# Kernel tuning notes

Hardware: AMD Instinct MI355X
Metric: run time of the kernel (lower is better)

## Reference

```python
import jax, jax.numpy as jnp
import numpy as np

N = 30000        # entities
R_EFF = 9        # 2*r+1 after enrich() with r=4
F_IN = 256       # insize
HID = 256        # hidden
NCLS = 32        # numcls
BASES = 16
E = 500000       # number of (enriched) triples / nonzeros


def setup_inputs() -> dict:
    key = jax.random.key(0)
    ks = jax.random.split(key, 8)
    features = jax.random.normal(ks[0], (N, F_IN), dtype=jnp.float32)
    # sparse vertical adjacency: entry at (rel*N + dst, src)
    ver_rows = jax.random.randint(ks[1], (E,), 0, R_EFF * N, dtype=jnp.int32)
    ver_cols = jax.random.randint(ks[2], (E,), 0, N, dtype=jnp.int32)
    # row-sum normalization (sum_sparse in the original): vals = 1 / row_degree
    deg = jax.ops.segment_sum(jnp.ones((E,), jnp.float32), ver_rows,
                              num_segments=R_EFF * N)
    ver_vals = 1.0 / deg[ver_rows]
    # xavier-uniform-ish params
    def xavier(k, shape):
        fan_in, fan_out = shape[-2], shape[-1]
        lim = jnp.sqrt(6.0 / (fan_in + fan_out)) * jnp.sqrt(2.0)  # relu gain
        return jax.random.uniform(k, shape, jnp.float32, -lim, lim)
    comps1 = xavier(ks[3], (R_EFF, BASES))
    bases1 = xavier(ks[4], (BASES, F_IN, HID))
    comps2 = xavier(ks[5], (R_EFF, BASES))
    bases2 = xavier(ks[6], (BASES, HID, NCLS))
    bias1 = jnp.zeros((HID,), jnp.float32)
    bias2 = jnp.zeros((NCLS,), jnp.float32)
    return {"features": features, "ver_vals": ver_vals,
            "comps1": comps1, "bases1": bases1,
            "comps2": comps2, "bases2": bases2,
            "bias1": bias1, "bias2": bias2,
            "ver_rows": ver_rows, "ver_cols": ver_cols}


def _spmm(vals, rows, cols, x, num_rows):
    # sparse [num_rows, n] @ x [n, d] -> [num_rows, d]
    msg = vals[:, None] * x[cols]          # (E, d) gather + scale
    return jax.ops.segment_sum(msg, rows, num_segments=num_rows)


def reference(features, ver_vals, comps1, bases1, comps2, bases2,
              bias1, bias2, ver_rows, ver_cols):
    n, f = features.shape
    r = comps1.shape[0]
    # layer 1: sparse aggregate, per-relation transform (basis decomp), sum over r
    h = _spmm(ver_vals, ver_rows, ver_cols, features, r * n)  # (r*n, f)
    h = h.reshape(r, n, f)
    w1 = jnp.einsum('rb,bfe->rfe', comps1, bases1)            # (r, f, hid)
    h = jnp.einsum('rnf,rfe->ne', h, w1)                      # bmm + sum over r
    h = jax.nn.relu(h + bias1)                                # (n, hid)
    # layer 2
    e = h.shape[1]
    h2 = _spmm(ver_vals, ver_rows, ver_cols, h, r * n).reshape(r, n, e)
    w2 = jnp.einsum('rb,bec->rec', comps2, bases2)            # (r, hid, ncls)
    out = jnp.einsum('rne,rec->nc', h2, w2) + bias2           # link_prediction=False
    return out
```

## Files before the change

### kernel.cpp

```cpp
#include <hip/hip_runtime.h>

typedef __attribute__((ext_vector_type(8))) short bf16x8;
typedef __attribute__((ext_vector_type(4))) float f32x4;

constexpr int NB = 16;
constexpr int REFF = 9;

struct alignas(8) EPair { float v; int c; };

__device__ __forceinline__ unsigned short f2bf(float f) {
  unsigned u = __float_as_uint(f);
  u += 0x7FFFu + ((u >> 16) & 1u);
  return (unsigned short)(u >> 16);
}
__device__ __forceinline__ float bflo(unsigned u) {
  return __uint_as_float(u << 16);
}
__device__ __forceinline__ float bfhi(unsigned u) {
  return __uint_as_float(u & 0xFFFF0000u);
}

__device__ __forceinline__ unsigned short pack_w_one(const float* __restrict__ comps,
                                                     const float* __restrict__ bases,
                                                     int idx, int NTI, int NTOT) {
  int j = idx & 7;
  int lane = (idx >> 3) & 63;
  int ni = (idx >> 9) % NTI;
  int t = (idx >> 9) / NTI;
  int ks = t & 7;
  int r = t >> 3;
  int k = ks * 32 + ((lane >> 4) << 3) + j;
  int n = ni * 16 + (lane & 15);
  float acc = 0.f;
#pragma unroll
  for (int b = 0; b < NB; ++b)
    acc += comps[r * NB + b] * bases[(size_t)b * 256 * NTOT + (size_t)k * NTOT + n];
  return f2bf(acc);
}

__global__ void hist_prep_kernel(const int* __restrict__ rows,
                                 int* __restrict__ deg1, int E,
                                 const float* __restrict__ features,
                                 unsigned short* __restrict__ Xbf,
                                 const float* __restrict__ comps1,
                                 const float* __restrict__ bases1,
                                 unsigned short* __restrict__ W1p,
                                 const float* __restrict__ comps2,
                                 const float* __restrict__ bases2,
                                 unsigned short* __restrict__ W2p, int N) {
  int idx = blockIdx.x * 256 + threadIdx.x;
  if (idx < E) atomicAdd(&deg1[rows[idx]], 1);
  const int n4 = N * 64;
  const int PW1 = REFF * 8 * 16 * 512;
  const int PW2 = REFF * 8 * 2 * 512;
  if (idx < n4) {
    float4 f = reinterpret_cast<const float4*>(features)[idx];
    ushort4 o;
    o.x = f2bf(f.x); o.y = f2bf(f.y); o.z = f2bf(f.z); o.w = f2bf(f.w);
    reinterpret_cast<ushort4*>(Xbf)[idx] = o;
  } else if (idx < n4 + PW1) {
    int i = idx - n4;
    W1p[i] = pack_w_one(comps1, bases1, i, 16, 256);
  } else if (idx < n4 + PW1 + PW2) {
    int i = idx - n4 - PW1;
    W2p[i] = pack_w_one(comps2, bases2, i, 2, 32);
  }
}

__global__ void scan1_kernel(const int* __restrict__ deg, int* __restrict__ bsum,
                             int NR) {
  __shared__ int s[256];
  int t = threadIdx.x;
  int base = blockIdx.x * 1024 + t * 4;
  int acc = 0;
#pragma unroll
  for (int q = 0; q < 4; ++q)
    if (base + q < NR) acc += deg[base + q];
  s[t] = acc;
  __syncthreads();
  for (int off = 128; off > 0; off >>= 1) {
    if (t < off) s[t] += s[t + off];
    __syncthreads();
  }
  if (t == 0) bsum[blockIdx.x] = s[0];
}

__global__ void scan2_kernel(int* __restrict__ bsum, int* __restrict__ ptr,
                             int NT, int NR) {
  __shared__ int s[512];
  int t = threadIdx.x;
  int v = (t < NT) ? bsum[t] : 0;
  s[t] = v;
  __syncthreads();
  for (int off = 1; off < 512; off <<= 1) {
    int x = (t >= off) ? s[t - off] : 0;
    __syncthreads();
    s[t] += x;
    __syncthreads();
  }
  if (t < NT) bsum[t] = s[t] - v;
  if (t == NT - 1) ptr[NR] = s[t];
}

__global__ void scan3_kernel(const int* __restrict__ deg,
                             const int* __restrict__ bsum,
                             int* __restrict__ ptr, int NR) {
  __shared__ int s[256];
  int t = threadIdx.x;
  int base = blockIdx.x * 1024 + t * 4;
  int d[4];
#pragma unroll
  for (int q = 0; q < 4; ++q)
    d[q] = (base + q < NR) ? deg[base + q] : 0;
  int tsum = d[0] + d[1] + d[2] + d[3];
  s[t] = tsum;
  __syncthreads();
  for (int off = 1; off < 256; off <<= 1) {
    int x = (t >= off) ? s[t - off] : 0;
    __syncthreads();
    s[t] += x;
    __syncthreads();
  }
  int off0 = bsum[blockIdx.x] + s[t] - tsum;
#pragma unroll
  for (int q = 0; q < 4; ++q) {
    if (base + q < NR) ptr[base + q] = off0;
    off0 += d[q];
  }
}

__global__ void fill_kernel(const int* __restrict__ rows,
                            const int* __restrict__ cols,
                            const float* __restrict__ vals,
                            int* __restrict__ deg1, const int* __restrict__ ptr1,
                            EPair* __restrict__ pay1, int E, int N) {
  int e = blockIdx.x * 256 + threadIdx.x;
  if (e >= E) return;
  int g = rows[e];
  int dst = g % N;
  int o1 = atomicSub(&deg1[g], 1);
  EPair pv; pv.v = vals[e]; pv.c = cols[e] | ((dst & 31) << 20);
  pay1[ptr1[g] + o1 - 1] = pv;
}

__global__ __launch_bounds__(512, 4)
void fused_l1(const EPair* __restrict__ pay1, const int* __restrict__ ptr1,
              const unsigned short* __restrict__ Xbf,
              const unsigned short* __restrict__ W1p,
              const float* __restrict__ bias1,
              const unsigned short* __restrict__ W2p,
              unsigned short* __restrict__ Y2, int N) {
  __shared__ char smem[34 * 1024];
  char* Xt   = smem;
  char* Mt   = smem + 16 * 1024;
  char* tile = smem + 18 * 1024;
  const int tid = threadIdx.x;
  const int w = tid >> 6, lane = tid & 63;
  const int l15 = lane & 15, kg = lane >> 4;
  const int node0 = blockIdx.x * 32;
  const int nrows = (N - node0 < 32) ? (N - node0) : 32;

  {
    uint4 z = make_uint4(0, 0, 0, 0);
    *reinterpret_cast<uint4*>(Xt + tid * 32) = z;
    *reinterpret_cast<uint4*>(Xt + tid * 32 + 16) = z;
  }
  __syncthreads();

  f32x4 acc[2][2];
#pragma unroll
  for (int mi = 0; mi < 2; ++mi)
#pragma unroll
    for (int ni = 0; ni < 2; ++ni) acc[mi][ni] = (f32x4)(0.f);

  const int sk = tid & 31;
  const int sn0 = (tid >> 5) << 4;

  for (int r = 0; r < REFF; ++r) {
    int g = r * N + node0;
    int s0 = ptr1[g], s1 = ptr1[g + nrows];
    int nch = (s1 - s0 + 31) >> 5;

    f32x4 agg[2][2];
#pragma unroll
    for (int mi = 0; mi < 2; ++mi)
#pragma unroll
      for (int ni = 0; ni < 2; ++ni) agg[mi][ni] = (f32x4)(0.f);

    EPair pe; bf16x8 px0, px1;
    {
      int rem = s1 - s0; if (rem > 32) rem = 32;
      if (sk < rem) {
        pe = pay1[s0 + sk];
        const unsigned short* xr = Xbf + (size_t)(pe.c & 0xFFFFF) * 256 + sn0;
        px0 = *reinterpret_cast<const bf16x8*>(xr);
        px1 = *reinterpret_cast<const bf16x8*>(xr + 8);
      }
    }

    for (int c = 0; c < nch; ++c) {
      int e0 = s0 + c * 32;
      int rem = s1 - e0; if (rem > 32) rem = 32;
      if (sk < rem) {
        int klo = sk & 7;
        int kgr = sk >> 3;
#pragma unroll
        for (int i = 0; i < 8; ++i) {
          int n = sn0 + i;
          int off = n * 64 + (((kgr ^ (n & 3)) << 3 | klo) << 1);
          *reinterpret_cast<unsigned short*>(Xt + off) = (unsigned short)px0[i];
        }
#pragma unroll
        for (int i = 0; i < 8; ++i) {
          int n = sn0 + 8 + i;
          int off = n * 64 + (((kgr ^ (n & 3)) << 3 | klo) << 1);
          *reinterpret_cast<unsigned short*>(Xt + off) = (unsigned short)px1[i];
        }
      }
      if (tid < 64) {
        uint4 z = make_uint4(0, 0, 0, 0);
        *reinterpret_cast<uint4*>(Mt + tid * 32) = z;
        *reinterpret_cast<uint4*>(Mt + tid * 32 + 16) = z;
      }
      if (tid < 32 && sk < rem) {
        int rr = (pe.c >> 20) & 31;
        int off = rr * 64 + (((((sk >> 3) ^ (rr & 3)) << 3) | (sk & 7)) << 1);
        *reinterpret_cast<unsigned short*>(Mt + off) = f2bf(pe.v);
      }
      __syncthreads();
      if (c + 1 < nch) {
        int e0n = e0 + 32;
        int remn = s1 - e0n; if (remn > 32) remn = 32;
        if (sk < remn) {
          pe = pay1[e0n + sk];
          const unsigned short* xr = Xbf + (size_t)(pe.c & 0xFFFFF) * 256 + sn0;
          px0 = *reinterpret_cast<const bf16x8*>(xr);
          px1 = *reinterpret_cast<const bf16x8*>(xr + 8);
        }
      }
      {
        int n_0 = w * 32 + l15;
        int n_1 = n_0 + 16;
        bf16x8 a0 = *reinterpret_cast<const bf16x8*>(
            Xt + n_0 * 64 + ((kg ^ (n_0 & 3)) << 4));
        bf16x8 a1 = *reinterpret_cast<const bf16x8*>(
            Xt + n_1 * 64 + ((kg ^ (n_1 & 3)) << 4));
        bf16x8 b0 = *reinterpret_cast<const bf16x8*>(
            Mt + l15 * 64 + ((kg ^ (l15 & 3)) << 4));
        bf16x8 b1 = *reinterpret_cast<const bf16x8*>(
            Mt + (l15 + 16) * 64 + ((kg ^ (l15 & 3)) << 4));
        agg[0][0] = __builtin_amdgcn_mfma_f32_16x16x32_bf16(a0, b0, agg[0][0], 0, 0, 0);
        agg[0][1] = __builtin_amdgcn_mfma_f32_16x16x32_bf16(a0, b1, agg[0][1], 0, 0, 0);
        agg[1][0] = __builtin_amdgcn_mfma_f32_16x16x32_bf16(a1, b0, agg[1][0], 0, 0, 0);
        agg[1][1] = __builtin_amdgcn_mfma_f32_16x16x32_bf16(a1, b1, agg[1][1], 0, 0, 0);
      }
      __syncthreads();
    }

#pragma unroll
    for (int mi = 0; mi < 2; ++mi)
#pragma unroll
      for (int ni = 0; ni < 2; ++ni)
#pragma unroll
        for (int reg = 0; reg < 4; ++reg) {
          int node = ni * 16 + l15;
          int n = w * 32 + mi * 16 + kg * 4 + reg;
          int byte = (node * 512 + n * 2) ^ ((node & 7) << 4);
          *reinterpret_cast<unsigned short*>(tile + byte) = f2bf(agg[mi][ni][reg]);
        }
    __syncthreads();
#pragma unroll 2
    for (int ks = 0; ks < 8; ++ks) {
      bf16x8 a[2];
#pragma unroll
      for (int mi = 0; mi < 2; ++mi) {
        int row = mi * 16 + l15;
        int boff = (row * 512 + ks * 64 + (kg << 4)) ^ ((row & 7) << 4);
        a[mi] = *reinterpret_cast<const bf16x8*>(tile + boff);
      }
#pragma unroll
      for (int ni = 0; ni < 2; ++ni) {
        int niG = w * 2 + ni;
        bf16x8 b = *reinterpret_cast<const bf16x8*>(
            W1p + (((size_t)(r * 8 + ks) * 16 + niG) << 9) + lane * 8);
#pragma unroll
        for (int mi = 0; mi < 2; ++mi)
          acc[mi][ni] = __builtin_amdgcn_mfma_f32_16x16x32_bf16(a[mi], b,
                                                               acc[mi][ni], 0, 0, 0);
      }
    }
    __syncthreads();
  }

#pragma unroll
  for (int mi = 0; mi < 2; ++mi) {
#pragma unroll
    for (int ni = 0; ni < 2; ++ni) {
      int col = (w * 2 + ni) * 16 + l15;
      float bb = bias1[col];
#pragma unroll
      for (int reg = 0; reg < 4; ++reg) {
        int row = mi * 16 + (kg << 2) + reg;
        float v = fmaxf(acc[mi][ni][reg] + bb, 0.f);
        int b = (row * 512 + col * 2) ^ ((row & 7) << 4);
        *reinterpret_cast<unsigned short*>(tile + b) = f2bf(v);
      }
    }
  }
  __syncthreads();

  unsigned short* ys = reinterpret_cast<unsigned short*>(Xt) + w * 1024;
  for (int rp = w; rp < REFF; rp += 8) {
    f32x4 a2[2][2];
#pragma unroll
    for (int mi = 0; mi < 2; ++mi) {
      a2[mi][0] = (f32x4)(0.f);
      a2[mi][1] = (f32x4)(0.f);
    }
#pragma unroll
    for (int ks = 0; ks < 8; ++ks) {
      bf16x8 b0 = *reinterpret_cast<const bf16x8*>(
          W2p + (((size_t)(rp * 8 + ks) * 2 + 0) << 9) + lane * 8);
      bf16x8 b1 = *reinterpret_cast<const bf16x8*>(
          W2p + (((size_t)(rp * 8 + ks) * 2 + 1) << 9) + lane * 8);
#pragma unroll
      for (int mi = 0; mi < 2; ++mi) {
        int row = mi * 16 + l15;
        int boff = (row * 512 + ks * 64 + (kg << 4)) ^ ((row & 7) << 4);
        bf16x8 a = *reinterpret_cast<const bf16x8*>(tile + boff);
        a2[mi][0] = __builtin_amdgcn_mfma_f32_16x16x32_bf16(a, b0, a2[mi][0], 0, 0, 0);
        a2[mi][1] = __builtin_amdgcn_mfma_f32_16x16x32_bf16(a, b1, a2[mi][1], 0, 0, 0);
      }
    }
#pragma unroll
    for (int mi = 0; mi < 2; ++mi)
#pragma unroll
      for (int reg = 0; reg < 4; ++reg) {
        int row16 = mi * 16 + (kg << 2) + reg;
        ys[row16 * 32 + l15] = f2bf(a2[mi][0][reg]);
        ys[row16 * 32 + 16 + l15] = f2bf(a2[mi][1][reg]);
      }
    asm volatile("s_waitcnt lgkmcnt(0)" ::: "memory");
#pragma unroll
    for (int half = 0; half < 2; ++half) {
      int row = half * 16 + (lane >> 2);
      int chunk = lane & 3;
      uint4 v = *reinterpret_cast<const uint4*>(&ys[row * 32 + chunk * 8]);
      int grow = node0 + row;
      if (grow < N)
        *reinterpret_cast<uint4*>(Y2 + (size_t)grow * (REFF * 32) + rp * 32 + chunk * 8) = v;
    }
  }
}

__global__ __launch_bounds__(512, 8)
void gather_out_kernel(const EPair* __restrict__ pay1,
                       const int* __restrict__ ptr1,
                       const unsigned short* __restrict__ Y2,
                       const float* __restrict__ bias2,
                       float* __restrict__ out, int N) {
  int wv = threadIdx.x >> 6;
  int lane = threadIdx.x & 63;
  int qw = lane >> 4, c = lane & 15;
  int n = blockIdx.x * 8 + wv;
  if (n >= N) return;
  float ax = 0.f, ay = 0.f;
  for (int r = qw; r < REFF; r += 4) {
    int g = r * N + n;
    int p0 = ptr1[g], p1 = ptr1[g + 1];
    int p = p0;
    for (; p + 2 <= p1; p += 2) {
      EPair e0 = pay1[p];
      EPair e1 = pay1[p + 1];
      unsigned u0 = *reinterpret_cast<const unsigned*>(
          Y2 + (size_t)(e0.c & 0xFFFFF) * (REFF * 32) + r * 32 + c * 2);
      unsigned u1 = *reinterpret_cast<const unsigned*>(
          Y2 + (size_t)(e1.c & 0xFFFFF) * (REFF * 32) + r * 32 + c * 2);
      ax += e0.v * bflo(u0) + e1.v * bflo(u1);
      ay += e0.v * bfhi(u0) + e1.v * bfhi(u1);
    }
    if (p < p1) {
      EPair e0 = pay1[p];
      unsigned u0 = *reinterpret_cast<const unsigned*>(
          Y2 + (size_t)(e0.c & 0xFFFFF) * (REFF * 32) + r * 32 + c * 2);
      ax += e0.v * bflo(u0);
      ay += e0.v * bfhi(u0);
    }
  }
  ax += __shfl_xor(ax, 16); ay += __shfl_xor(ay, 16);
  ax += __shfl_xor(ax, 32); ay += __shfl_xor(ay, 32);
  if (lane < 16) {
    float2 o;
    o.x = ax + bias2[c * 2];
    o.y = ay + bias2[c * 2 + 1];
    reinterpret_cast<float2*>(out)[(size_t)n * 16 + c] = o;
  }
}

extern "C" void kernel_launch(void* const* d_in, const int* in_sizes, int n_in,
                              void* d_out, int out_size, void* d_ws, size_t ws_size,
                              hipStream_t stream) {
  const float* features = (const float*)d_in[0];
  const float* ver_vals = (const float*)d_in[1];
  const float* comps1   = (const float*)d_in[2];
  const float* bases1   = (const float*)d_in[3];
  const float* comps2   = (const float*)d_in[4];
  const float* bases2   = (const float*)d_in[5];
  const float* bias1    = (const float*)d_in[6];
  const float* bias2    = (const float*)d_in[7];
  const int* ver_rows   = (const int*)d_in[8];
  const int* ver_cols   = (const int*)d_in[9];

  const int N = in_sizes[0] / 256;
  const int E = in_sizes[1];
  const int NR = REFF * N;
  const int NT = (NR + 1023) / 1024;

  char* p = (char*)d_ws;
  unsigned short* Xbf = (unsigned short*)p; p += (size_t)N * 256 * 2;
  unsigned short* Y2  = (unsigned short*)p; p += (size_t)N * REFF * 32 * 2;
  unsigned short* W1p = (unsigned short*)p; p += (size_t)REFF * 65536 * 2;
  unsigned short* W2p = (unsigned short*)p; p += (size_t)REFF * 8192 * 2;
  int* ptr1 = (int*)p;     p += (size_t)(NR + 4) * 4;
  EPair* pay1 = (EPair*)p; p += (size_t)E * 8;
  int* deg1 = (int*)p;     p += (size_t)NR * 4;
  int* bsum = (int*)p;     p += 512 * 4;

  hipMemsetAsync(deg1, 0, (size_t)NR * 4, stream);
  const int prep_total = N * 64 + REFF * 8 * 16 * 512 + REFF * 8 * 2 * 512;
  const int hp_grid = ((prep_total > E ? prep_total : E) + 255) / 256;
  hist_prep_kernel<<<hp_grid, 256, 0, stream>>>(ver_rows, deg1, E,
                                                features, Xbf,
                                                comps1, bases1, W1p,
                                                comps2, bases2, W2p, N);
  scan1_kernel<<<NT, 256, 0, stream>>>(deg1, bsum, NR);
  scan2_kernel<<<1, 512, 0, stream>>>(bsum, ptr1, NT, NR);
  scan3_kernel<<<NT, 256, 0, stream>>>(deg1, bsum, ptr1, NR);
  fill_kernel<<<(E + 255) / 256, 256, 0, stream>>>(ver_rows, ver_cols, ver_vals,
                                                   deg1, ptr1, pay1, E, N);

  fused_l1<<<(N + 31) / 32, 512, 0, stream>>>(pay1, ptr1, Xbf, W1p, bias1,
                                              W2p, Y2, N);
  gather_out_kernel<<<(N + 7) / 8, 512, 0, stream>>>(pay1, ptr1, Y2, bias2,
                                                     (float*)d_out, N);
}
```

Before: 222.5 us.

## Give each wave private LDS staging so edge-chunk aggregation runs without block barriers

Each of the 8 waves now owns its own transposed feature tile and message tile in shared memory and handles a 32-column slice, so the per-chunk __syncthreads pair in the sparse aggregation loop is removed. The first chunk of the next relation is prefetched before the per-relation dense GEMM, and a new swizzle replaces the old bank-conflict pattern. Each wave now redundantly loads the edge payloads and builds its own message matrix. Shared memory grows from 34 KB to 48 KB, which may limit occupancy.

Result: slower. 228.0 us (+2.5%).

```diff
diff --git a/kernel.cpp b/kernel.cpp
--- a/kernel.cpp
+++ b/kernel.cpp
@@ -18,6 +18,9 @@
 }
 __device__ __forceinline__ float bfhi(unsigned u) {
   return __uint_as_float(u & 0xFFFF0000u);
+}
+__device__ __forceinline__ int swz(int row) {
+  return ((row & 7) << 4) ^ ((row & 16) << 1);
 }
 
 __device__ __forceinline__ unsigned short pack_w_one(const float* __restrict__ comps,
@@ -150,22 +153,23 @@
               const float* __restrict__ bias1,
               const unsigned short* __restrict__ W2p,
               unsigned short* __restrict__ Y2, int N) {
-  __shared__ char smem[34 * 1024];
-  char* Xt   = smem;
-  char* Mt   = smem + 16 * 1024;
-  char* tile = smem + 18 * 1024;
+  __shared__ char smem[48 * 1024];
   const int tid = threadIdx.x;
   const int w = tid >> 6, lane = tid & 63;
   const int l15 = lane & 15, kg = lane >> 4;
+  char* Xw   = smem + w * 2048;
+  char* Mw   = smem + 16 * 1024 + w * 2048;
+  char* tile = smem + 32 * 1024;
+
   const int node0 = blockIdx.x * 32;
   const int nrows = (N - node0 < 32) ? (N - node0) : 32;
+  const int e = lane & 31, h = lane >> 5;
 
   {
     uint4 z = make_uint4(0, 0, 0, 0);
-    *reinterpret_cast<uint4*>(Xt + tid * 32) = z;
-    *reinterpret_cast<uint4*>(Xt + tid * 32 + 16) = z;
-  }
-  __syncthreads();
+    *reinterpret_cast<uint4*>(smem + tid * 32) = z;
+    *reinterpret_cast<uint4*>(smem + tid * 32 + 16) = z;
+  }
 
   f32x4 acc[2][2];
 #pragma unroll
@@ -173,102 +177,102 @@
 #pragma unroll
     for (int ni = 0; ni < 2; ++ni) acc[mi][ni] = (f32x4)(0.f);
 
-  const int sk = tid & 31;
-  const int sn0 = (tid >> 5) << 4;
+  int s0 = ptr1[node0], s1 = ptr1[node0 + nrows];
+  EPair pe; bf16x8 px0, px1;
+  {
+    int rem = s1 - s0; if (rem > 32) rem = 32;
+    if (e < rem) {
+      pe = pay1[s0 + e];
+      const unsigned short* xr = Xbf + (size_t)(pe.c & 0xFFFFF) * 256 + w * 32 + h * 16;
+      px0 = *reinterpret_cast<const bf16x8*>(xr);
+      px1 = *reinterpret_cast<const bf16x8*>(xr + 8);
+    }
+  }
 
   for (int r = 0; r < REFF; ++r) {
-    int g = r * N + node0;
-    int s0 = ptr1[g], s1 = ptr1[g + nrows];
     int nch = (s1 - s0 + 31) >> 5;
-
     f32x4 agg[2][2];
 #pragma unroll
     for (int mi = 0; mi < 2; ++mi)
 #pragma unroll
       for (int ni = 0; ni < 2; ++ni) agg[mi][ni] = (f32x4)(0.f);
 
-    EPair pe; bf16x8 px0, px1;
-    {
-      int rem = s1 - s0; if (rem > 32) rem = 32;
-      if (sk < rem) {
-        pe = pay1[s0 + sk];
-        const unsigned short* xr = Xbf + (size_t)(pe.c & 0xFFFFF) * 256 + sn0;
-        px0 = *reinterpret_cast<const bf16x8*>(xr);
-        px1 = *reinterpret_cast<const bf16x8*>(xr + 8);
-      }
-    }
-
     for (int c = 0; c < nch; ++c) {
-      int e0 = s0 + c * 32;
-      int rem = s1 - e0; if (rem > 32) rem = 32;
-      if (sk < rem) {
-        int klo = sk & 7;
-        int kgr = sk >> 3;
+      int rem = s1 - (s0 + c * 32); if (rem > 32) rem = 32;
+      if (e < rem) {
 #pragma unroll
         for (int i = 0; i < 8; ++i) {
-          int n = sn0 + i;
-          int off = n * 64 + (((kgr ^ (n & 3)) << 3 | klo) << 1);
-          *reinterpret_cast<unsigned short*>(Xt + off) = (unsigned short)px0[i];
+          int np = h * 16 + i;
+          *reinterpret_cast<unsigned short*>(Xw + ((np * 64 + e * 2) ^ swz(np))) =
+              (unsigned short)px0[i];
         }
 #pragma unroll
         for (int i = 0; i < 8; ++i) {
-          int n = sn0 + 8 + i;
-          int off = n * 64 + (((kgr ^ (n & 3)) << 3 | klo) << 1);
-          *reinterpret_cast<unsigned short*>(Xt + off) = (unsigned short)px1[i];
+          int np = h * 16 + 8 + i;
+          *reinterpret_cast<unsigned short*>(Xw + ((np * 64 + e * 2) ^ swz(np))) =
+              (unsigned short)px1[i];
         }
       }
-      if (tid < 64) {
+      {
         uint4 z = make_uint4(0, 0, 0, 0);
-        *reinterpret_cast<uint4*>(Mt + tid * 32) = z;
-        *reinterpret_cast<uint4*>(Mt + tid * 32 + 16) = z;
-      }
-      if (tid < 32 && sk < rem) {
+        *reinterpret_cast<uint4*>(Mw + lane * 32) = z;
+        *reinterpret_cast<uint4*>(Mw + lane * 32 + 16) = z;
+      }
+      if (h == 0 && e < rem) {
         int rr = (pe.c >> 20) & 31;
-        int off = rr * 64 + (((((sk >> 3) ^ (rr & 3)) << 3) | (sk & 7)) << 1);
-        *reinterpret_cast<unsigned short*>(Mt + off) = f2bf(pe.v);
-      }
-      __syncthreads();
+        *reinterpret_cast<unsigned short*>(Mw + ((rr * 64 + e * 2) ^ swz(rr))) =
+            f2bf(pe.v);
+      }
       if (c + 1 < nch) {
-        int e0n = e0 + 32;
-        int remn = s1 - e0n; if (remn > 32) remn = 32;
-        if (sk < remn) {
-          pe = pay1[e0n + sk];
-          const unsigned short* xr = Xbf + (size_t)(pe.c & 0xFFFFF) * 256 + sn0;
+        int remn = s1 - (s0 + (c + 1) * 32); if (remn > 32) remn = 32;
+        if (e < remn) {
+          pe = pay1[s0 + (c + 1) * 32 + e];
+          const unsigned short* xr = Xbf + (size_t)(pe.c & 0xFFFFF) * 256 + w * 32 + h * 16;
           px0 = *reinterpret_cast<const bf16x8*>(xr);
           px1 = *reinterpret_cast<const bf16x8*>(xr + 8);
         }
       }
       {
-        int n_0 = w * 32 + l15;
-        int n_1 = n_0 + 16;
         bf16x8 a0 = *reinterpret_cast<const bf16x8*>(
-            Xt + n_0 * 64 + ((kg ^ (n_0 & 3)) << 4));
+            Xw + ((l15 * 64 + kg * 16) ^ swz(l15)));
         bf16x8 a1 = *reinterpret_cast<const bf16x8*>(
-            Xt + n_1 * 64 + ((kg ^ (n_1 & 3)) << 4));
+            Xw + (((l15 + 16) * 64 + kg * 16) ^ swz(l15 + 16)));
         bf16x8 b0 = *reinterpret_cast<const bf16x8*>(
-            Mt + l15 * 64 + ((kg ^ (l15 & 3)) << 4));
+            Mw + ((l15 * 64 + kg * 16) ^ swz(l15)));
         bf16x8 b1 = *reinterpret_cast<const bf16x8*>(
-            Mt + (l15 + 16) * 64 + ((kg ^ (l15 & 3)) << 4));
+            Mw + (((l15 + 16) * 64 + kg * 16) ^ swz(l15 + 16)));
         agg[0][0] = __builtin_amdgcn_mfma_f32_16x16x32_bf16(a0, b0, agg[0][0], 0, 0, 0);
         agg[0][1] = __builtin_amdgcn_mfma_f32_16x16x32_bf16(a0, b1, agg[0][1], 0, 0, 0);
         agg[1][0] = __builtin_amdgcn_mfma_f32_16x16x32_bf16(a1, b0, agg[1][0], 0, 0, 0);
         agg[1][1] = __builtin_amdgcn_mfma_f32_16x16x32_bf16(a1, b1, agg[1][1], 0, 0, 0);
       }
-      __syncthreads();
     }
 
 #pragma unroll
     for (int mi = 0; mi < 2; ++mi)
 #pragma unroll
-      for (int ni = 0; ni < 2; ++ni)
+      for (int nj = 0; nj < 2; ++nj)
 #pragma unroll
         for (int reg = 0; reg < 4; ++reg) {
-          int node = ni * 16 + l15;
+          int node = nj * 16 + l15;
           int n = w * 32 + mi * 16 + kg * 4 + reg;
           int byte = (node * 512 + n * 2) ^ ((node & 7) << 4);
-          *reinterpret_cast<unsigned short*>(tile + byte) = f2bf(agg[mi][ni][reg]);
+          *reinterpret_cast<unsigned short*>(tile + byte) = f2bf(agg[mi][nj][reg]);
         }
     __syncthreads();
+
+    if (r + 1 < REFF) {
+      s0 = ptr1[(r + 1) * N + node0];
+      s1 = ptr1[(r + 1) * N + node0 + nrows];
+      int rem = s1 - s0; if (rem > 32) rem = 32;
+      if (e < rem) {
+        pe = pay1[s0 + e];
+        const unsigned short* xr = Xbf + (size_t)(pe.c & 0xFFFFF) * 256 + w * 32 + h * 16;
+        px0 = *reinterpret_cast<const bf16x8*>(xr);
+        px1 = *reinterpret_cast<const bf16x8*>(xr + 8);
+      }
+    }
+
 #pragma unroll 2
     for (int ks = 0; ks < 8; ++ks) {
       bf16x8 a[2];
@@ -309,7 +313,7 @@
   }
   __syncthreads();
 
-  unsigned short* ys = reinterpret_cast<unsigned short*>(Xt) + w * 1024;
+  unsigned short* ys = reinterpret_cast<unsigned short*>(Xw);
   for (int rp = w; rp < REFF; rp += 8) {
     f32x4 a2[2][2];
 #pragma unroll
```
